# Optimization experiments

Hardware: AMD Instinct MI355X
Metric: run time of the kernel (lower is better)

The kernel has to match this reference:

```python
import jax, jax.numpy as jnp
import numpy as np

D = 1024
H = 16
HD = D // H
DS = 64
B, L = 2, 2048


def setup_inputs() -> dict:
    key = jax.random.key(0)
    ks = jax.random.split(key, 12)
    s = 0.02
    return {
        "x": jax.random.normal(ks[0], (B, L, D), jnp.float32),
        "subject_embed": jax.random.normal(ks[1], (B, DS), jnp.float32),
        "key_padding_mask": jnp.zeros((B, L), jnp.bool_),
        "Wq": jax.random.normal(ks[2], (D, D), jnp.float32) * s,
        "Wk": jax.random.normal(ks[3], (D, D), jnp.float32) * s,
        "Wv": jax.random.normal(ks[4], (D, D), jnp.float32) * s,
        "Wo": jax.random.normal(ks[5], (D, D), jnp.float32) * s,
        "bo": jnp.zeros((D,), jnp.float32),
        "Wsq": jax.random.normal(ks[6], (DS, D), jnp.float32) * s,
        "bsq": jnp.zeros((D,), jnp.float32),
        "Wsk": jax.random.normal(ks[7], (DS, D), jnp.float32) * s,
        "bsk": jnp.zeros((D,), jnp.float32),
    }


def reference(x, subject_embed, key_padding_mask, Wq, Wk, Wv, Wo, bo, Wsq, bsq, Wsk, bsk):
    scale = 1.0 / jnp.sqrt(jnp.asarray(HD, x.dtype))
    q = x @ Wq + (subject_embed @ Wsq + bsq)[:, None, :]   # [B,L,D]
    k = x @ Wk + (subject_embed @ Wsk + bsk)[:, None, :]
    v = x @ Wv
    # split heads: [B,H,L,hd]
    q = q.reshape(B, L, H, HD).transpose(0, 2, 1, 3)
    k = k.reshape(B, L, H, HD).transpose(0, 2, 1, 3)
    v = v.reshape(B, L, H, HD).transpose(0, 2, 1, 3)
    attn = jnp.einsum('bhqd,bhkd->bhqk', q, k) * scale      # [B,H,L,L]
    attn = jnp.where(key_padding_mask[:, None, None, :], -jnp.inf, attn)
    attn = jax.nn.softmax(attn, axis=-1)
    out = jnp.einsum('bhqk,bhkd->bhqd', attn, v)
    out = out.transpose(0, 2, 1, 3).reshape(B, L, D)
    return out @ Wo + bo
```

## Files before the change

### kernel.cpp

```cpp
#include <hip/hip_runtime.h>
#include <hip/hip_bf16.h>
#include <math.h>

#define DEV __device__ __forceinline__

typedef short bf16x8 __attribute__((ext_vector_type(8)));
typedef float f32x4 __attribute__((ext_vector_type(4)));

static constexpr int D  = 1024;
static constexpr int H  = 16;
static constexpr int HD = 64;
static constexpr int DS = 64;
static constexpr int B  = 2;
static constexpr int L  = 2048;
static constexpr int M  = B * L;

static constexpr float QSCALE = 0.18033688011112042f;

DEV unsigned short f2bf(float f) {
  union { float f; unsigned u; } x; x.f = f;
  unsigned r = (x.u + 0x7FFFu + ((x.u >> 16) & 1u)) >> 16;
  return (unsigned short)r;
}

DEV unsigned pack2bf(float a, float b) {
  return (unsigned)f2bf(a) | ((unsigned)f2bf(b) << 16);
}

DEV unsigned pack2bf_trunc(float a, float b) {
  union { float f; unsigned u; } ua{a}, ub{b};
  return (ua.u >> 16) | (ub.u & 0xffff0000u);
}

DEV void gload_lds16(const void* g, void* l) {
  __builtin_amdgcn_global_load_lds(
      (const __attribute__((address_space(1))) unsigned int*)g,
      (__attribute__((address_space(3))) unsigned int*)l, 16, 0, 0);
}

__global__ __launch_bounds__(256) void prep_kernel(
    const float* __restrict__ Wq, const float* __restrict__ Wk,
    const float* __restrict__ Wv, const float* __restrict__ Wo,
    const float* __restrict__ x, const float* __restrict__ subj,
    const float* __restrict__ Wsq, const float* __restrict__ bsq,
    const float* __restrict__ Wsk, const float* __restrict__ bsk,
    unsigned short* __restrict__ WT4, unsigned short* __restrict__ xb,
    float* __restrict__ sq, float* __restrict__ sk) {
  __shared__ float tile[64][65];
  const int blk = blockIdx.x, t = threadIdx.x;
  if (blk < 1024) {
    const int z = blk >> 8, idx = blk & 255;
    const float* W = z == 0 ? Wq : z == 1 ? Wk : z == 2 ? Wv : Wo;
    unsigned short* dst = WT4 + (size_t)z * D * D;
    const int n0 = (idx & 15) * 64, k0 = (idx >> 4) * 64;
    const int c = t & 63, r4 = t >> 6;
#pragma unroll
    for (int rr = 0; rr < 16; ++rr) {
      int row = r4 + rr * 4;
      tile[row][c] = W[(size_t)(k0 + row) * D + n0 + c];
    }
    __syncthreads();
#pragma unroll
    for (int rr = 0; rr < 16; ++rr) {
      int nrow = r4 + rr * 4;
      dst[(size_t)(n0 + nrow) * D + k0 + c] = f2bf(tile[c][nrow]);
    }
  } else if (blk < 3072) {
    size_t g = (size_t)(blk - 1024) * 256 + t;
    const float4* xf = (const float4*)x;
    float4 a = xf[2 * g], b = xf[2 * g + 1];
    union { unsigned short s[8]; uint4 v; } o;
    o.s[0] = f2bf(a.x); o.s[1] = f2bf(a.y); o.s[2] = f2bf(a.z); o.s[3] = f2bf(a.w);
    o.s[4] = f2bf(b.x); o.s[5] = f2bf(b.y); o.s[6] = f2bf(b.z); o.s[7] = f2bf(b.w);
    ((uint4*)xb)[g] = o.v;
  } else {
    int g = (blk - 3072) * 256 + t;
    int ty = g >> 11, b = (g >> 10) & 1, n = g & 1023;
    const float* W = ty ? Wsk : Wsq;
    const float* bias = ty ? bsk : bsq;
    float s = bias[n];
#pragma unroll 8
    for (int d = 0; d < DS; ++d) s += subj[b * DS + d] * W[d * D + n];
    (ty ? sk : sq)[b * D + n] = s;
  }
}

__global__ __launch_bounds__(256) void proj_kernel(
    const unsigned short* __restrict__ xb, const unsigned short* __restrict__ WT3,
    const float* __restrict__ sq, const float* __restrict__ sk,
    unsigned short* __restrict__ qk, unsigned short* __restrict__ vT) {
  __shared__ __align__(16) unsigned short smem[128 * 136];
  unsigned short* As = smem;
  unsigned short* Bs = smem + 128 * 64;
  const int z = blockIdx.z;
  const unsigned short* Wt = WT3 + (size_t)z * D * D;
  const int m0 = blockIdx.y * 128, n0 = blockIdx.x * 128;
  const int t = threadIdx.x, l = t & 63, w = t >> 6;
  const int wm = w >> 1, wn = w & 1;
  const int lm = l & 15, lq = l >> 4;
  const int srow8 = t >> 3;
  const int fsw = ((t & 7) ^ ((t >> 3) & 7)) * 8;
  const int swm = lm & 7;
  f32x4 acc[4][4] = {};
  for (int kt = 0; kt < D / 64; ++kt) {
    const int kb = kt * 64;
#pragma unroll
    for (int c = 0; c < 4; ++c) {
      int row = 32 * c + srow8;
      gload_lds16(&xb[(size_t)(m0 + row) * D + kb + fsw], &As[(32 * c + 8 * w) * 64]);
      gload_lds16(&Wt[(size_t)(n0 + row) * D + kb + fsw], &Bs[(32 * c + 8 * w) * 64]);
    }
    __syncthreads();
#pragma unroll
    for (int kk = 0; kk < 2; ++kk) {
      bf16x8 af[4], bf[4];
#pragma unroll
      for (int i = 0; i < 4; ++i)
        af[i] = *(const bf16x8*)&As[(64 * wm + 16 * i + lm) * 64 + ((kk * 4 + lq) ^ swm) * 8];
#pragma unroll
      for (int j = 0; j < 4; ++j)
        bf[j] = *(const bf16x8*)&Bs[(64 * wn + 16 * j + lm) * 64 + ((kk * 4 + lq) ^ swm) * 8];
#pragma unroll
      for (int i = 0; i < 4; ++i)
#pragma unroll
        for (int j = 0; j < 4; ++j)
          acc[i][j] = __builtin_amdgcn_mfma_f32_16x16x32_bf16(af[i], bf[j], acc[i][j], 0, 0, 0);
    }
    __syncthreads();
  }
  if (z == 2) {
#pragma unroll
    for (int i = 0; i < 4; ++i)
#pragma unroll
      for (int j = 0; j < 4; ++j) {
        int cr = 64 * wn + 16 * j + lm;
        int rr = 64 * wm + 16 * i + 4 * lq;
        uint2 u;
        u.x = pack2bf(acc[i][j][0], acc[i][j][1]);
        u.y = pack2bf(acc[i][j][2], acc[i][j][3]);
        *(uint2*)&smem[cr * 136 + rr] = u;
      }
    __syncthreads();
    const int cr = t >> 1, half = t & 1;
    const int bb = m0 >> 11, l0 = m0 & (L - 1);
    const int gcol = n0 + cr, h = gcol >> 6, hd = gcol & 63;
    size_t dbase = ((size_t)(bb * H + h) * HD + hd) * L + l0 + half * 64;
#pragma unroll
    for (int c = 0; c < 8; ++c) {
      uint4 u = *(const uint4*)&smem[cr * 136 + half * 64 + c * 8];
      *(uint4*)&vT[dbase + c * 8] = u;
    }
  } else {
    unsigned short* dst = qk + (size_t)z * M * D;
    const float* bias = z == 0 ? sq : sk;
    const float post = z == 0 ? QSCALE : 1.0f;
#pragma unroll
    for (int i = 0; i < 4; ++i)
#pragma unroll
      for (int j = 0; j < 4; ++j)
#pragma unroll
        for (int r = 0; r < 4; ++r) {
          int grow = m0 + 64 * wm + 16 * i + lq * 4 + r;
          int gcol = n0 + 64 * wn + 16 * j + lm;
          int bb = grow >> 11, ll = grow & (L - 1);
          float v = (acc[i][j][r] + bias[bb * D + gcol]) * post;
          int h = gcol >> 6, hd = gcol & 63;
          dst[((size_t)(bb * H + h) * L + ll) * HD + hd] = f2bf(v);
        }
  }
}

__global__ __launch_bounds__(256) void attn_kernel(
    const unsigned short* __restrict__ q_hm, const unsigned short* __restrict__ k_hm,
    const unsigned short* __restrict__ vT, const unsigned char* __restrict__ mask,
    unsigned short* __restrict__ ctx) {
  __shared__ unsigned short Ksb[2 * 64 * 64];
  __shared__ unsigned short Vtb[2 * 64 * 64];
  __shared__ unsigned short Ps[128 * 72];
  const int bx = blockIdx.x;
  const int rest = bx >> 3;
  const int bhid = (bx & 7) + 8 * (rest >> 4);
  const int q0 = (rest & 15) * 128;
  const int h = bhid & 15, b = bhid >> 4;
  const size_t bh = (size_t)(b * H + h);
  const unsigned short* qp = q_hm + bh * L * HD;
  const unsigned short* kp = k_hm + bh * L * HD;
  const unsigned short* vp = vT + bh * HD * L;
  const int t = threadIdx.x, l = t & 63, w = t >> 6;
  const int lm = l & 15, lq = l >> 4;
  const int fsw = ((t & 7) ^ ((t >> 3) & 7)) * 8;
  const int swm = lm & 7;
  const int srow = t >> 3;

  unsigned short* Qs = Ps;
#pragma unroll
  for (int c = 0; c < 4; ++c) {
    int row = 32 * c + srow;
    gload_lds16(&qp[(size_t)(q0 + row) * HD + fsw], &Qs[(32 * c + 8 * w) * 64]);
  }
#pragma unroll
  for (int c = 0; c < 2; ++c) {
    int row = 32 * c + srow;
    gload_lds16(&kp[(size_t)row * HD + fsw], &Ksb[(32 * c + 8 * w) * 64]);
    gload_lds16(&vp[(size_t)row * L + fsw], &Vtb[(32 * c + 8 * w) * 64]);
  }
  __syncthreads();
  bf16x8 qf[2][2];
#pragma unroll
  for (int i = 0; i < 2; ++i)
#pragma unroll
    for (int kk = 0; kk < 2; ++kk)
      qf[i][kk] = *(const bf16x8*)&Qs[(w * 32 + 16 * i + lm) * 64 + ((kk * 4 + lq) ^ swm) * 8];

  float lsum[2] = {0.f, 0.f};
  f32x4 ot[4][2] = {};

  for (int kt = 0; kt < L / 64; ++kt) {
    const int cur = kt & 1;
    const unsigned short* Kc = Ksb + cur * (64 * 64);
    const unsigned short* Vc = Vtb + cur * (64 * 64);
    if (kt + 1 < L / 64) {
      const int nk0 = (kt + 1) * 64;
      unsigned short* Kd = Ksb + (cur ^ 1) * (64 * 64);
      unsigned short* Vd = Vtb + (cur ^ 1) * (64 * 64);
#pragma unroll
      for (int c = 0; c < 2; ++c) {
        int row = 32 * c + srow;
        gload_lds16(&kp[(size_t)(nk0 + row) * HD + fsw], &Kd[(32 * c + 8 * w) * 64]);
        gload_lds16(&vp[(size_t)row * L + nk0 + fsw], &Vd[(32 * c + 8 * w) * 64]);
      }
    }
    unsigned long long mb = __ballot(mask[b * L + kt * 64 + l] != 0);

    f32x4 st[4][2];
#pragma unroll
    for (int jt = 0; jt < 4; ++jt) {
      bf16x8 kf[2];
#pragma unroll
      for (int kk = 0; kk < 2; ++kk)
        kf[kk] = *(const bf16x8*)&Kc[(16 * jt + lm) * 64 + ((kk * 4 + lq) ^ swm) * 8];
#pragma unroll
      for (int i = 0; i < 2; ++i) {
        f32x4 a = {};
        a = __builtin_amdgcn_mfma_f32_16x16x32_bf16(kf[0], qf[i][0], a, 0, 0, 0);
        a = __builtin_amdgcn_mfma_f32_16x16x32_bf16(kf[1], qf[i][1], a, 0, 0, 0);
        st[jt][i] = a;
      }
    }
    if (mb) {
      unsigned mlo = (unsigned)(mb >> (4 * lq));
      unsigned mhi = (unsigned)(mb >> (4 * lq + 32));
#pragma unroll
      for (int jt = 0; jt < 4; ++jt)
#pragma unroll
        for (int i = 0; i < 2; ++i)
#pragma unroll
          for (int r = 0; r < 4; ++r) {
            unsigned bits = jt < 2 ? mlo : mhi;
            if ((bits >> (16 * (jt & 1) + r)) & 1u) st[jt][i][r] = -1e30f;
          }
    }
#pragma unroll
    for (int i = 0; i < 2; ++i) {
      float ps = 0.f;
#pragma unroll
      for (int jt = 0; jt < 4; ++jt) {
        f32x4 p;
#pragma unroll
        for (int r = 0; r < 4; ++r) {
          float e = __builtin_amdgcn_exp2f(st[jt][i][r]);
          p[r] = e;
          ps += e;
        }
        uint2 u;
        u.x = pack2bf_trunc(p[0], p[1]);
        u.y = pack2bf_trunc(p[2], p[3]);
        *(uint2*)&Ps[(w * 32 + 16 * i + lm) * 72 + 16 * jt + 4 * lq] = u;
      }
      lsum[i] += ps;
    }
    bf16x8 pf[2][2];
#pragma unroll
    for (int i = 0; i < 2; ++i)
#pragma unroll
      for (int kk = 0; kk < 2; ++kk)
        pf[i][kk] = *(const bf16x8*)&Ps[(w * 32 + 16 * i + lm) * 72 + kk * 32 + lq * 8];
#pragma unroll
    for (int jf = 0; jf < 4; ++jf) {
      bf16x8 vf[2];
#pragma unroll
      for (int kk = 0; kk < 2; ++kk)
        vf[kk] = *(const bf16x8*)&Vc[(16 * jf + lm) * 64 + ((kk * 4 + lq) ^ swm) * 8];
#pragma unroll
      for (int i = 0; i < 2; ++i) {
        ot[jf][i] = __builtin_amdgcn_mfma_f32_16x16x32_bf16(vf[0], pf[i][0], ot[jf][i], 0, 0, 0);
        ot[jf][i] = __builtin_amdgcn_mfma_f32_16x16x32_bf16(vf[1], pf[i][1], ot[jf][i], 0, 0, 0);
      }
    }
    __syncthreads();
  }

  float rl[2];
#pragma unroll
  for (int i = 0; i < 2; ++i) {
    float s = lsum[i];
    s += __shfl_xor(s, 16, 64);
    s += __shfl_xor(s, 32, 64);
    rl[i] = 1.0f / s;
  }

#pragma unroll
  for (int i = 0; i < 2; ++i) {
#pragma unroll
    for (int jf = 0; jf < 4; ++jf) {
      uint2 u;
      u.x = pack2bf(ot[jf][i][0] * rl[i], ot[jf][i][1] * rl[i]);
      u.y = pack2bf(ot[jf][i][2] * rl[i], ot[jf][i][3] * rl[i]);
      *(uint2*)&Ps[(w * 32 + 16 * i + lm) * 72 + 16 * jf + 4 * lq] = u;
    }
  }
  {
    int row = l >> 1, half = l & 1;
    size_t obase = ((size_t)(b * L + q0 + w * 32 + row)) * D + h * HD + half * 32;
#pragma unroll
    for (int c = 0; c < 4; ++c) {
      uint4 u = *(const uint4*)&Ps[(w * 32 + row) * 72 + half * 32 + c * 8];
      *(uint4*)&ctx[obase + c * 8] = u;
    }
  }
}

__global__ __launch_bounds__(256) void outgemm_kernel(
    const unsigned short* __restrict__ ctx, const unsigned short* __restrict__ WoT,
    const float* __restrict__ bo, float* __restrict__ out) {
  __shared__ unsigned short As[64 * 64];
  __shared__ unsigned short Bs[128 * 64];
  const int m0 = blockIdx.y * 64, n0 = blockIdx.x * 128;
  const int t = threadIdx.x, l = t & 63, w = t >> 6;
  const int wm = w >> 1, wn = w & 1;
  const int lm = l & 15, lq = l >> 4;
  const int srow8 = t >> 3;
  const int fsw = ((t & 7) ^ ((t >> 3) & 7)) * 8;
  const int swm = lm & 7;
  f32x4 acc[2][4] = {};
  for (int kt = 0; kt < D / 64; ++kt) {
    const int kb = kt * 64;
#pragma unroll
    for (int c = 0; c < 2; ++c)
      gload_lds16(&ctx[(size_t)(m0 + 32 * c + srow8) * D + kb + fsw],
                  &As[(32 * c + 8 * w) * 64]);
#pragma unroll
    for (int c = 0; c < 4; ++c)
      gload_lds16(&WoT[(size_t)(n0 + 32 * c + srow8) * D + kb + fsw],
                  &Bs[(32 * c + 8 * w) * 64]);
    __syncthreads();
#pragma unroll
    for (int kk = 0; kk < 2; ++kk) {
      bf16x8 af[2], bf[4];
#pragma unroll
      for (int i = 0; i < 2; ++i)
        af[i] = *(const bf16x8*)&As[(32 * wm + 16 * i + lm) * 64 + ((kk * 4 + lq) ^ swm) * 8];
#pragma unroll
      for (int j = 0; j < 4; ++j)
        bf[j] = *(const bf16x8*)&Bs[(64 * wn + 16 * j + lm) * 64 + ((kk * 4 + lq) ^ swm) * 8];
#pragma unroll
      for (int i = 0; i < 2; ++i)
#pragma unroll
        for (int j = 0; j < 4; ++j)
          acc[i][j] = __builtin_amdgcn_mfma_f32_16x16x32_bf16(af[i], bf[j], acc[i][j], 0, 0, 0);
    }
    __syncthreads();
  }
#pragma unroll
  for (int i = 0; i < 2; ++i)
#pragma unroll
    for (int j = 0; j < 4; ++j)
#pragma unroll
      for (int r = 0; r < 4; ++r) {
        int grow = m0 + 32 * wm + 16 * i + lq * 4 + r;
        int gcol = n0 + 64 * wn + 16 * j + lm;
        out[(size_t)grow * D + gcol] = acc[i][j][r] + bo[gcol];
      }
}

extern "C" void kernel_launch(void* const* d_in, const int* in_sizes, int n_in,
                              void* d_out, int out_size, void* d_ws, size_t ws_size,
                              hipStream_t stream) {
  const float* x    = (const float*)d_in[0];
  const float* subj = (const float*)d_in[1];
  const unsigned char* mask = (const unsigned char*)d_in[2];
  const float* Wq = (const float*)d_in[3];
  const float* Wk = (const float*)d_in[4];
  const float* Wv = (const float*)d_in[5];
  const float* Wo = (const float*)d_in[6];
  const float* bo = (const float*)d_in[7];
  const float* Wsq = (const float*)d_in[8];
  const float* bsq = (const float*)d_in[9];
  const float* Wsk = (const float*)d_in[10];
  const float* bsk = (const float*)d_in[11];
  float* out = (float*)d_out;
  char* ws = (char*)d_ws;

  unsigned short* xb  = (unsigned short*)(ws);
  unsigned short* WT4 = (unsigned short*)(ws + (8ull  << 20));
  unsigned short* qk  = (unsigned short*)(ws + (16ull << 20));
  unsigned short* ctx = (unsigned short*)(ws + (32ull << 20));
  unsigned short* vT  = (unsigned short*)(ws + (40ull << 20));
  float* sq = (float*)(ws + (48ull << 20));
  float* sk = sq + B * D;

  hipLaunchKernelGGL(prep_kernel, dim3(3088), dim3(256), 0, stream,
                     Wq, Wk, Wv, Wo, x, subj, Wsq, bsq, Wsk, bsk, WT4, xb, sq, sk);
  hipLaunchKernelGGL(proj_kernel, dim3(8, 32, 3), dim3(256), 0, stream,
                     xb, WT4, sq, sk, qk, vT);
  hipLaunchKernelGGL(attn_kernel, dim3(512), dim3(256), 0, stream,
                     qk, qk + (size_t)M * D, vT, mask, ctx);
  hipLaunchKernelGGL(outgemm_kernel, dim3(8, 64, 1), dim3(256), 0, stream, ctx,
                     WT4 + 3ull * D * D, bo, out);
}
```

Before: 218.8 us.

## Split attention KV range in two and merge partials in a reduce kernel

The attention kernel now splits each query tile's key range into two halves, doubling the grid so more blocks are resident per CU. Each half writes unnormalized bf16 partial outputs and row sums to workspace. A new reduce kernel adds the two partials, normalizes them and writes the context tensor. This costs extra global traffic for the partials, an extra launch, and some precision from storing unnormalized partials in bf16.

```diff
diff --git a/kernel.cpp b/kernel.cpp
--- a/kernel.cpp
+++ b/kernel.cpp
@@ -21,6 +21,10 @@
   union { float f; unsigned u; } x; x.f = f;
   unsigned r = (x.u + 0x7FFFu + ((x.u >> 16) & 1u)) >> 16;
   return (unsigned short)r;
+}
+
+DEV float bf2f(unsigned short s) {
+  union { unsigned u; float f; } x; x.u = (unsigned)s << 16; return x.f;
 }
 
 DEV unsigned pack2bf(float a, float b) {
@@ -173,16 +177,19 @@
 __global__ __launch_bounds__(256) void attn_kernel(
     const unsigned short* __restrict__ q_hm, const unsigned short* __restrict__ k_hm,
     const unsigned short* __restrict__ vT, const unsigned char* __restrict__ mask,
-    unsigned short* __restrict__ ctx) {
+    unsigned short* __restrict__ opart, float* __restrict__ lsp) {
   __shared__ unsigned short Ksb[2 * 64 * 64];
   __shared__ unsigned short Vtb[2 * 64 * 64];
   __shared__ unsigned short Ps[128 * 72];
   const int bx = blockIdx.x;
   const int rest = bx >> 3;
-  const int bhid = (bx & 7) + 8 * (rest >> 4);
-  const int q0 = (rest & 15) * 128;
+  const int bhid = (bx & 7) + 8 * (rest >> 5);
+  const int qs = rest & 31;
+  const int q0 = (qs >> 1) * 128;
+  const int split = qs & 1;
   const int h = bhid & 15, b = bhid >> 4;
   const size_t bh = (size_t)(b * H + h);
+  const int slot = ((bhid * 16 + (qs >> 1)) * 2 + split);
   const unsigned short* qp = q_hm + bh * L * HD;
   const unsigned short* kp = k_hm + bh * L * HD;
   const unsigned short* vp = vT + bh * HD * L;
@@ -191,6 +198,7 @@
   const int fsw = ((t & 7) ^ ((t >> 3) & 7)) * 8;
   const int swm = lm & 7;
   const int srow = t >> 3;
+  const int kt0 = split * (L / 128), kt1 = kt0 + L / 128;
 
   unsigned short* Qs = Ps;
 #pragma unroll
@@ -201,8 +209,8 @@
 #pragma unroll
   for (int c = 0; c < 2; ++c) {
     int row = 32 * c + srow;
-    gload_lds16(&kp[(size_t)row * HD + fsw], &Ksb[(32 * c + 8 * w) * 64]);
-    gload_lds16(&vp[(size_t)row * L + fsw], &Vtb[(32 * c + 8 * w) * 64]);
+    gload_lds16(&kp[(size_t)(kt0 * 64 + row) * HD + fsw], &Ksb[(32 * c + 8 * w) * 64]);
+    gload_lds16(&vp[(size_t)row * L + kt0 * 64 + fsw], &Vtb[(32 * c + 8 * w) * 64]);
   }
   __syncthreads();
   bf16x8 qf[2][2];
@@ -215,11 +223,11 @@
   float lsum[2] = {0.f, 0.f};
   f32x4 ot[4][2] = {};
 
-  for (int kt = 0; kt < L / 64; ++kt) {
+  for (int kt = kt0; kt < kt1; ++kt) {
     const int cur = kt & 1;
     const unsigned short* Kc = Ksb + cur * (64 * 64);
     const unsigned short* Vc = Vtb + cur * (64 * 64);
-    if (kt + 1 < L / 64) {
+    if (kt + 1 < kt1) {
       const int nk0 = (kt + 1) * 64;
       unsigned short* Kd = Ksb + (cur ^ 1) * (64 * 64);
       unsigned short* Vd = Vtb + (cur ^ 1) * (64 * 64);
@@ -300,33 +308,47 @@
     __syncthreads();
   }
 
-  float rl[2];
+  unsigned short* op = opart + (size_t)slot * (128 * 64);
 #pragma unroll
   for (int i = 0; i < 2; ++i) {
     float s = lsum[i];
     s += __shfl_xor(s, 16, 64);
     s += __shfl_xor(s, 32, 64);
-    rl[i] = 1.0f / s;
-  }
-
-#pragma unroll
-  for (int i = 0; i < 2; ++i) {
 #pragma unroll
     for (int jf = 0; jf < 4; ++jf) {
       uint2 u;
-      u.x = pack2bf(ot[jf][i][0] * rl[i], ot[jf][i][1] * rl[i]);
-      u.y = pack2bf(ot[jf][i][2] * rl[i], ot[jf][i][3] * rl[i]);
-      *(uint2*)&Ps[(w * 32 + 16 * i + lm) * 72 + 16 * jf + 4 * lq] = u;
-    }
-  }
-  {
-    int row = l >> 1, half = l & 1;
-    size_t obase = ((size_t)(b * L + q0 + w * 32 + row)) * D + h * HD + half * 32;
-#pragma unroll
-    for (int c = 0; c < 4; ++c) {
-      uint4 u = *(const uint4*)&Ps[(w * 32 + row) * 72 + half * 32 + c * 8];
-      *(uint4*)&ctx[obase + c * 8] = u;
-    }
+      u.x = pack2bf(ot[jf][i][0], ot[jf][i][1]);
+      u.y = pack2bf(ot[jf][i][2], ot[jf][i][3]);
+      *(uint2*)&op[(w * 32 + 16 * i + lm) * 64 + 16 * jf + 4 * lq] = u;
+    }
+    if (l < 16) lsp[slot * 128 + w * 32 + 16 * i + l] = s;
+  }
+}
+
+__global__ __launch_bounds__(256) void reduce_kernel(
+    const unsigned short* __restrict__ opart, const float* __restrict__ lsp,
+    unsigned short* __restrict__ ctx) {
+  const int qt = blockIdx.x, bh = blockIdx.y;
+  const int t = threadIdx.x, row = t >> 1, half = t & 1;
+  const int slot = (bh * 16 + qt) * 2;
+  const unsigned short* o0 = opart + (size_t)slot * (128 * 64);
+  const unsigned short* o1 = o0 + 128 * 64;
+  const float rl = 1.0f / (lsp[slot * 128 + row] + lsp[(slot + 1) * 128 + row]);
+  const int b = bh >> 4, h = bh & 15;
+  size_t cb = ((size_t)(b * L + qt * 128 + row)) * D + h * 64 + half * 32;
+#pragma unroll
+  for (int c = 0; c < 4; ++c) {
+    int off = row * 64 + half * 32 + c * 8;
+    union { uint4 v; unsigned short s[8]; } u0, u1, o;
+    u0.v = *(const uint4*)&o0[off];
+    u1.v = *(const uint4*)&o1[off];
+#pragma unroll
+    for (int e = 0; e < 8; e += 2) {
+      float a = (bf2f(u0.s[e]) + bf2f(u1.s[e])) * rl;
+      float bb2 = (bf2f(u0.s[e + 1]) + bf2f(u1.s[e + 1])) * rl;
+      ((unsigned*)&o.v)[e >> 1] = pack2bf(a, bb2);
+    }
+    *(uint4*)&ctx[cb + c * 8] = o.v;
   }
 }
 
@@ -401,20 +423,24 @@
   float* out = (float*)d_out;
   char* ws = (char*)d_ws;
 
-  unsigned short* xb  = (unsigned short*)(ws);
-  unsigned short* WT4 = (unsigned short*)(ws + (8ull  << 20));
-  unsigned short* qk  = (unsigned short*)(ws + (16ull << 20));
-  unsigned short* ctx = (unsigned short*)(ws + (32ull << 20));
-  unsigned short* vT  = (unsigned short*)(ws + (40ull << 20));
-  float* sq = (float*)(ws + (48ull << 20));
-  float* sk = sq + B * D;
+  unsigned short* xb    = (unsigned short*)(ws);
+  unsigned short* WT4   = (unsigned short*)(ws + (8ull  << 20));
+  unsigned short* qk    = (unsigned short*)(ws + (16ull << 20));
+  unsigned short* ctx   = (unsigned short*)(ws + (32ull << 20));
+  unsigned short* vT    = (unsigned short*)(ws + (40ull << 20));
+  float* sq             = (float*)(ws + (48ull << 20));
+  float* sk             = sq + B * D;
+  unsigned short* opart = (unsigned short*)(ws + (49ull << 20));
+  float* lsp            = (float*)(ws + (65ull << 20));
 
   hipLaunchKernelGGL(prep_kernel, dim3(3088), dim3(256), 0, stream,
                      Wq, Wk, Wv, Wo, x, subj, Wsq, bsq, Wsk, bsk, WT4, xb, sq, sk);
   hipLaunchKernelGGL(proj_kernel, dim3(8, 32, 3), dim3(256), 0, stream,
                      xb, WT4, sq, sk, qk, vT);
-  hipLaunchKernelGGL(attn_kernel, dim3(512), dim3(256), 0, stream,
-                     qk, qk + (size_t)M * D, vT, mask, ctx);
+  hipLaunchKernelGGL(attn_kernel, dim3(1024), dim3(256), 0, stream,
+                     qk, qk + (size_t)M * D, vT, mask, opart, lsp);
+  hipLaunchKernelGGL(reduce_kernel, dim3(16, 32), dim3(256), 0, stream,
+                     opart, lsp, ctx);
   hipLaunchKernelGGL(outgemm_kernel, dim3(8, 64, 1), dim3(256), 0, stream, ctx,
                      WT4 + 3ull * D * D, bo, out);
 }
```

New measurement: 228.3 us. 4.3% more time.

## Keep softmax probabilities in registers for PV MFMA and stage Q/K epilogue via LDS

Applied to the files above, without the earlier changes.

The attention PV product now uses 16x16x16 bf16 MFMA with the probability tile taken straight from registers as the A operand. This removes the per-tile LDS write and read-back of P, with the output accumulator transposed to match. The Q/K projection epilogue now stages results in shared memory and writes coalesced 16-byte rows in head-major layout instead of scattered 2-byte stores. The trade-off is twice as many smaller MFMA instructions and narrower V loads from LDS, plus an extra barrier in the GEMM epilogue.

```diff
diff --git a/kernel.cpp b/kernel.cpp
--- a/kernel.cpp
+++ b/kernel.cpp
@@ -5,7 +5,14 @@
 #define DEV __device__ __forceinline__
 
 typedef short bf16x8 __attribute__((ext_vector_type(8)));
+typedef short bf16x4 __attribute__((ext_vector_type(4)));
 typedef float f32x4 __attribute__((ext_vector_type(4)));
+
+#if __has_builtin(__builtin_amdgcn_mfma_f32_16x16x16bf16_1k)
+#define HAVE_MFMA16 1
+#else
+#define HAVE_MFMA16 0
+#endif
 
 static constexpr int D  = 1024;
 static constexpr int H  = 16;
@@ -160,13 +167,21 @@
       for (int j = 0; j < 4; ++j)
 #pragma unroll
         for (int r = 0; r < 4; ++r) {
-          int grow = m0 + 64 * wm + 16 * i + lq * 4 + r;
-          int gcol = n0 + 64 * wn + 16 * j + lm;
-          int bb = grow >> 11, ll = grow & (L - 1);
-          float v = (acc[i][j][r] + bias[bb * D + gcol]) * post;
-          int h = gcol >> 6, hd = gcol & 63;
-          dst[((size_t)(bb * H + h) * L + ll) * HD + hd] = f2bf(v);
+          int rr = 64 * wm + 16 * i + 4 * lq + r;
+          int cc = 64 * wn + 16 * j + lm;
+          float v = (acc[i][j][r] + bias[((m0 + rr) >> 11) * D + n0 + cc]) * post;
+          smem[rr * 136 + cc] = f2bf(v);
         }
+    __syncthreads();
+    const int row = t >> 1, half = t & 1;
+    const int bb = m0 >> 11, ll = (m0 & (L - 1)) + row;
+    const int h0 = (n0 >> 6) + half;
+    size_t dbase = ((size_t)(bb * H + h0) * L + ll) * HD;
+#pragma unroll
+    for (int c = 0; c < 8; ++c) {
+      uint4 u = *(const uint4*)&smem[row * 136 + half * 64 + c * 8];
+      *(uint4*)&dst[dbase + c * 8] = u;
+    }
   }
 }
 
@@ -213,7 +228,7 @@
       qf[i][kk] = *(const bf16x8*)&Qs[(w * 32 + 16 * i + lm) * 64 + ((kk * 4 + lq) ^ swm) * 8];
 
   float lsum[2] = {0.f, 0.f};
-  f32x4 ot[4][2] = {};
+  f32x4 ot[2][4] = {};
 
   for (int kt = 0; kt < L / 64; ++kt) {
     const int cur = kt & 1;
@@ -260,6 +275,9 @@
             if ((bits >> (16 * (jt & 1) + r)) & 1u) st[jt][i][r] = -1e30f;
           }
     }
+#if HAVE_MFMA16
+    union { uint2 u; bf16x4 v; } pp[2][4];
+#endif
 #pragma unroll
     for (int i = 0; i < 2; ++i) {
       float ps = 0.f;
@@ -272,13 +290,32 @@
           p[r] = e;
           ps += e;
         }
+#if HAVE_MFMA16
+        pp[i][jt].u.x = pack2bf_trunc(p[0], p[1]);
+        pp[i][jt].u.y = pack2bf_trunc(p[2], p[3]);
+#else
         uint2 u;
         u.x = pack2bf_trunc(p[0], p[1]);
         u.y = pack2bf_trunc(p[2], p[3]);
         *(uint2*)&Ps[(w * 32 + 16 * i + lm) * 72 + 16 * jt + 4 * lq] = u;
+#endif
       }
       lsum[i] += ps;
     }
+#if HAVE_MFMA16
+#pragma unroll
+    for (int jf = 0; jf < 4; ++jf) {
+#pragma unroll
+      for (int kc = 0; kc < 4; ++kc) {
+        int chunk = (2 * kc + (lq >> 1)) ^ swm;
+        bf16x4 vb = *(const bf16x4*)&Vc[(16 * jf + lm) * 64 + chunk * 8 + 4 * (lq & 1)];
+#pragma unroll
+        for (int i = 0; i < 2; ++i)
+          ot[i][jf] = __builtin_amdgcn_mfma_f32_16x16x16bf16_1k(
+              pp[i][kc].v, vb, ot[i][jf], 0, 0, 0);
+      }
+    }
+#else
     bf16x8 pf[2][2];
 #pragma unroll
     for (int i = 0; i < 2; ++i)
@@ -293,10 +330,11 @@
         vf[kk] = *(const bf16x8*)&Vc[(16 * jf + lm) * 64 + ((kk * 4 + lq) ^ swm) * 8];
 #pragma unroll
       for (int i = 0; i < 2; ++i) {
-        ot[jf][i] = __builtin_amdgcn_mfma_f32_16x16x32_bf16(vf[0], pf[i][0], ot[jf][i], 0, 0, 0);
-        ot[jf][i] = __builtin_amdgcn_mfma_f32_16x16x32_bf16(vf[1], pf[i][1], ot[jf][i], 0, 0, 0);
-      }
-    }
+        ot[i][jf] = __builtin_amdgcn_mfma_f32_16x16x32_bf16(vf[0], pf[i][0], ot[i][jf], 0, 0, 0);
+        ot[i][jf] = __builtin_amdgcn_mfma_f32_16x16x32_bf16(vf[1], pf[i][1], ot[i][jf], 0, 0, 0);
+      }
+    }
+#endif
     __syncthreads();
   }
 
@@ -309,16 +347,30 @@
     rl[i] = 1.0f / s;
   }
 
+#if HAVE_MFMA16
 #pragma unroll
   for (int i = 0; i < 2; ++i) {
+    float rlq[4];
+#pragma unroll
+    for (int r = 0; r < 4; ++r) rlq[r] = __shfl(rl[i], 4 * lq + r, 64);
+#pragma unroll
+    for (int jf = 0; jf < 4; ++jf)
+#pragma unroll
+      for (int r = 0; r < 4; ++r)
+        Ps[(w * 32 + 16 * i + 4 * lq + r) * 72 + 16 * jf + lm] =
+            f2bf(ot[i][jf][r] * rlq[r]);
+  }
+#else
+#pragma unroll
+  for (int i = 0; i < 2; ++i)
 #pragma unroll
     for (int jf = 0; jf < 4; ++jf) {
       uint2 u;
-      u.x = pack2bf(ot[jf][i][0] * rl[i], ot[jf][i][1] * rl[i]);
-      u.y = pack2bf(ot[jf][i][2] * rl[i], ot[jf][i][3] * rl[i]);
+      u.x = pack2bf(ot[i][jf][0] * rl[i], ot[i][jf][1] * rl[i]);
+      u.y = pack2bf(ot[i][jf][2] * rl[i], ot[i][jf][3] * rl[i]);
       *(uint2*)&Ps[(w * 32 + 16 * i + lm) * 72 + 16 * jf + 4 * lq] = u;
     }
-  }
+#endif
   {
     int row = l >> 1, half = l & 1;
     size_t obase = ((size_t)(b * L + q0 + w * 32 + row)) * D + h * HD + half * 32;
```

Result: no change. 220.5 us (+0.8%).

## Keep softmax probabilities in registers for PV MFMA and widen key tiles

Applied to the files above, without the earlier changes.

The attention kernel now feeds the exp'd score fragments straight into a 16x16x16 MFMA as the A operand, which removes the LDS round-trip for P. Key tiles grow from 64 to 128 rows, halving the loop iterations and barriers, and the V tile layout and swizzle change to suit the new operand order. The QK projection epilogue also stages results through shared memory so head-major writes become coalesced 16-byte stores. The cost is more LDS per block (larger K/V double buffers), which may reduce occupancy, plus extra shuffles to redistribute the row normalisers in the epilogue.

```diff
diff --git a/kernel.cpp b/kernel.cpp
--- a/kernel.cpp
+++ b/kernel.cpp
@@ -5,6 +5,7 @@
 #define DEV __device__ __forceinline__
 
 typedef short bf16x8 __attribute__((ext_vector_type(8)));
+typedef short bf16x4 __attribute__((ext_vector_type(4)));
 typedef float f32x4 __attribute__((ext_vector_type(4)));
 
 static constexpr int D  = 1024;
@@ -160,13 +161,21 @@
       for (int j = 0; j < 4; ++j)
 #pragma unroll
         for (int r = 0; r < 4; ++r) {
-          int grow = m0 + 64 * wm + 16 * i + lq * 4 + r;
-          int gcol = n0 + 64 * wn + 16 * j + lm;
-          int bb = grow >> 11, ll = grow & (L - 1);
-          float v = (acc[i][j][r] + bias[bb * D + gcol]) * post;
-          int h = gcol >> 6, hd = gcol & 63;
-          dst[((size_t)(bb * H + h) * L + ll) * HD + hd] = f2bf(v);
+          int rr = 64 * wm + 16 * i + 4 * lq + r;
+          int cc = 64 * wn + 16 * j + lm;
+          float v = (acc[i][j][r] + bias[((m0 + rr) >> 11) * D + n0 + cc]) * post;
+          smem[rr * 136 + cc] = f2bf(v);
         }
+    __syncthreads();
+    const int row = t >> 1, half = t & 1;
+    const int bb = m0 >> 11, ll = (m0 & (L - 1)) + row;
+    const int h0 = (n0 >> 6) + half;
+    size_t dbase = ((size_t)(bb * H + h0) * L + ll) * HD;
+#pragma unroll
+    for (int c = 0; c < 8; ++c) {
+      uint4 u = *(const uint4*)&smem[row * 136 + half * 64 + c * 8];
+      *(uint4*)&dst[dbase + c * 8] = u;
+    }
   }
 }
 
@@ -174,9 +183,9 @@
     const unsigned short* __restrict__ q_hm, const unsigned short* __restrict__ k_hm,
     const unsigned short* __restrict__ vT, const unsigned char* __restrict__ mask,
     unsigned short* __restrict__ ctx) {
-  __shared__ unsigned short Ksb[2 * 64 * 64];
-  __shared__ unsigned short Vtb[2 * 64 * 64];
-  __shared__ unsigned short Ps[128 * 72];
+  __shared__ unsigned short Qs[128 * 64];
+  __shared__ unsigned short Ksb[2 * 128 * 64];
+  __shared__ unsigned short Vtb[2 * 64 * 128];
   const int bx = blockIdx.x;
   const int rest = bx >> 3;
   const int bhid = (bx & 7) + 8 * (rest >> 4);
@@ -191,18 +200,14 @@
   const int fsw = ((t & 7) ^ ((t >> 3) & 7)) * 8;
   const int swm = lm & 7;
   const int srow = t >> 3;
-
-  unsigned short* Qs = Ps;
+  const int vs = t & 15, vr = t >> 4;
+  const int vcsrc = ((vs & 8) | ((vs & 7) ^ (vr & 7))) * 8;
+
 #pragma unroll
   for (int c = 0; c < 4; ++c) {
-    int row = 32 * c + srow;
-    gload_lds16(&qp[(size_t)(q0 + row) * HD + fsw], &Qs[(32 * c + 8 * w) * 64]);
-  }
-#pragma unroll
-  for (int c = 0; c < 2; ++c) {
-    int row = 32 * c + srow;
-    gload_lds16(&kp[(size_t)row * HD + fsw], &Ksb[(32 * c + 8 * w) * 64]);
-    gload_lds16(&vp[(size_t)row * L + fsw], &Vtb[(32 * c + 8 * w) * 64]);
+    gload_lds16(&qp[(size_t)(q0 + 32 * c + srow) * HD + fsw], &Qs[(32 * c + 8 * w) * 64]);
+    gload_lds16(&kp[(size_t)(32 * c + srow) * HD + fsw], &Ksb[(32 * c + 8 * w) * 64]);
+    gload_lds16(&vp[(size_t)(16 * c + vr) * L + vcsrc], &Vtb[(16 * c + 4 * w) * 128]);
   }
   __syncthreads();
   bf16x8 qf[2][2];
@@ -213,88 +218,73 @@
       qf[i][kk] = *(const bf16x8*)&Qs[(w * 32 + 16 * i + lm) * 64 + ((kk * 4 + lq) ^ swm) * 8];
 
   float lsum[2] = {0.f, 0.f};
-  f32x4 ot[4][2] = {};
-
-  for (int kt = 0; kt < L / 64; ++kt) {
+  f32x4 ot[2][4] = {};
+
+  for (int kt = 0; kt < L / 128; ++kt) {
     const int cur = kt & 1;
-    const unsigned short* Kc = Ksb + cur * (64 * 64);
-    const unsigned short* Vc = Vtb + cur * (64 * 64);
-    if (kt + 1 < L / 64) {
-      const int nk0 = (kt + 1) * 64;
-      unsigned short* Kd = Ksb + (cur ^ 1) * (64 * 64);
-      unsigned short* Vd = Vtb + (cur ^ 1) * (64 * 64);
-#pragma unroll
-      for (int c = 0; c < 2; ++c) {
-        int row = 32 * c + srow;
-        gload_lds16(&kp[(size_t)(nk0 + row) * HD + fsw], &Kd[(32 * c + 8 * w) * 64]);
-        gload_lds16(&vp[(size_t)row * L + nk0 + fsw], &Vd[(32 * c + 8 * w) * 64]);
-      }
-    }
-    unsigned long long mb = __ballot(mask[b * L + kt * 64 + l] != 0);
-
-    f32x4 st[4][2];
-#pragma unroll
-    for (int jt = 0; jt < 4; ++jt) {
-      bf16x8 kf[2];
-#pragma unroll
-      for (int kk = 0; kk < 2; ++kk)
-        kf[kk] = *(const bf16x8*)&Kc[(16 * jt + lm) * 64 + ((kk * 4 + lq) ^ swm) * 8];
+    const unsigned short* Kc = Ksb + cur * (128 * 64);
+    const unsigned short* Vc = Vtb + cur * (64 * 128);
+    unsigned char mby0 = mask[b * L + kt * 128 + l];
+    unsigned char mby1 = mask[b * L + kt * 128 + 64 + l];
+    if (kt + 1 < L / 128) {
+      const int nk0 = (kt + 1) * 128;
+      unsigned short* Kd = Ksb + (cur ^ 1) * (128 * 64);
+      unsigned short* Vd = Vtb + (cur ^ 1) * (64 * 128);
+#pragma unroll
+      for (int c = 0; c < 4; ++c) {
+        gload_lds16(&kp[(size_t)(nk0 + 32 * c + srow) * HD + fsw], &Kd[(32 * c + 8 * w) * 64]);
+        gload_lds16(&vp[(size_t)(16 * c + vr) * L + nk0 + vcsrc], &Vd[(16 * c + 4 * w) * 128]);
+      }
+    }
+    unsigned long long mb0 = __ballot(mby0 != 0);
+    unsigned long long mb1 = __ballot(mby1 != 0);
+
+#pragma unroll
+    for (int jt = 0; jt < 8; ++jt) {
+      bf16x8 kf0 = *(const bf16x8*)&Kc[(16 * jt + lm) * 64 + ((0 + lq) ^ swm) * 8];
+      bf16x8 kf1 = *(const bf16x8*)&Kc[(16 * jt + lm) * 64 + ((4 + lq) ^ swm) * 8];
+      f32x4 st[2];
 #pragma unroll
       for (int i = 0; i < 2; ++i) {
         f32x4 a = {};
-        a = __builtin_amdgcn_mfma_f32_16x16x32_bf16(kf[0], qf[i][0], a, 0, 0, 0);
-        a = __builtin_amdgcn_mfma_f32_16x16x32_bf16(kf[1], qf[i][1], a, 0, 0, 0);
-        st[jt][i] = a;
-      }
-    }
-    if (mb) {
-      unsigned mlo = (unsigned)(mb >> (4 * lq));
-      unsigned mhi = (unsigned)(mb >> (4 * lq + 32));
-#pragma unroll
-      for (int jt = 0; jt < 4; ++jt)
+        a = __builtin_amdgcn_mfma_f32_16x16x32_bf16(kf0, qf[i][0], a, 0, 0, 0);
+        a = __builtin_amdgcn_mfma_f32_16x16x32_bf16(kf1, qf[i][1], a, 0, 0, 0);
+        st[i] = a;
+      }
+      unsigned long long mbX = jt < 4 ? mb0 : mb1;
+      if (mbX) {
+        int jm = jt & 3;
+        unsigned bits = (unsigned)(mbX >> (4 * lq + 16 * jm));
 #pragma unroll
         for (int i = 0; i < 2; ++i)
 #pragma unroll
-          for (int r = 0; r < 4; ++r) {
-            unsigned bits = jt < 2 ? mlo : mhi;
-            if ((bits >> (16 * (jt & 1) + r)) & 1u) st[jt][i][r] = -1e30f;
-          }
-    }
-#pragma unroll
-    for (int i = 0; i < 2; ++i) {
-      float ps = 0.f;
-#pragma unroll
-      for (int jt = 0; jt < 4; ++jt) {
+          for (int r = 0; r < 4; ++r)
+            if ((bits >> r) & 1u) st[i][r] = -1e30f;
+      }
+      union { uint2 u; bf16x4 v; } pp[2];
+#pragma unroll
+      for (int i = 0; i < 2; ++i) {
         f32x4 p;
+        float ps = 0.f;
 #pragma unroll
         for (int r = 0; r < 4; ++r) {
-          float e = __builtin_amdgcn_exp2f(st[jt][i][r]);
+          float e = __builtin_amdgcn_exp2f(st[i][r]);
           p[r] = e;
           ps += e;
         }
-        uint2 u;
-        u.x = pack2bf_trunc(p[0], p[1]);
-        u.y = pack2bf_trunc(p[2], p[3]);
-        *(uint2*)&Ps[(w * 32 + 16 * i + lm) * 72 + 16 * jt + 4 * lq] = u;
-      }
-      lsum[i] += ps;
-    }
-    bf16x8 pf[2][2];
-#pragma unroll
-    for (int i = 0; i < 2; ++i)
-#pragma unroll
-      for (int kk = 0; kk < 2; ++kk)
-        pf[i][kk] = *(const bf16x8*)&Ps[(w * 32 + 16 * i + lm) * 72 + kk * 32 + lq * 8];
-#pragma unroll
-    for (int jf = 0; jf < 4; ++jf) {
-      bf16x8 vf[2];
-#pragma unroll
-      for (int kk = 0; kk < 2; ++kk)
-        vf[kk] = *(const bf16x8*)&Vc[(16 * jf + lm) * 64 + ((kk * 4 + lq) ^ swm) * 8];
-#pragma unroll
-      for (int i = 0; i < 2; ++i) {
-        ot[jf][i] = __builtin_amdgcn_mfma_f32_16x16x32_bf16(vf[0], pf[i][0], ot[jf][i], 0, 0, 0);
-        ot[jf][i] = __builtin_amdgcn_mfma_f32_16x16x32_bf16(vf[1], pf[i][1], ot[jf][i], 0, 0, 0);
+        lsum[i] += ps;
+        pp[i].u.x = pack2bf_trunc(p[0], p[1]);
+        pp[i].u.y = pack2bf_trunc(p[2], p[3]);
+      }
+      const int kc2 = 2 * jt + (lq >> 1);
+      const int slot = (kc2 & 8) | ((kc2 & 7) ^ swm);
+#pragma unroll
+      for (int jf = 0; jf < 4; ++jf) {
+        bf16x4 vb = *(const bf16x4*)&Vc[(16 * jf + lm) * 128 + slot * 8 + 4 * (lq & 1)];
+#pragma unroll
+        for (int i = 0; i < 2; ++i)
+          ot[i][jf] = __builtin_amdgcn_mfma_f32_16x16x16bf16_1k(
+              pp[i].v, vb, ot[i][jf], 0, 0, 0);
       }
     }
     __syncthreads();
@@ -309,22 +299,25 @@
     rl[i] = 1.0f / s;
   }
 
+  unsigned short* Es = Ksb;
 #pragma unroll
   for (int i = 0; i < 2; ++i) {
-#pragma unroll
-    for (int jf = 0; jf < 4; ++jf) {
-      uint2 u;
-      u.x = pack2bf(ot[jf][i][0] * rl[i], ot[jf][i][1] * rl[i]);
-      u.y = pack2bf(ot[jf][i][2] * rl[i], ot[jf][i][3] * rl[i]);
-      *(uint2*)&Ps[(w * 32 + 16 * i + lm) * 72 + 16 * jf + 4 * lq] = u;
-    }
+    float rlq[4];
+#pragma unroll
+    for (int r = 0; r < 4; ++r) rlq[r] = __shfl(rl[i], 4 * lq + r, 64);
+#pragma unroll
+    for (int jf = 0; jf < 4; ++jf)
+#pragma unroll
+      for (int r = 0; r < 4; ++r)
+        Es[(w * 32 + 16 * i + 4 * lq + r) * 72 + 16 * jf + lm] =
+            f2bf(ot[i][jf][r] * rlq[r]);
   }
   {
     int row = l >> 1, half = l & 1;
     size_t obase = ((size_t)(b * L + q0 + w * 32 + row)) * D + h * HD + half * 32;
 #pragma unroll
     for (int c = 0; c < 4; ++c) {
-      uint4 u = *(const uint4*)&Ps[(w * 32 + row) * 72 + half * 32 + c * 8];
+      uint4 u = *(const uint4*)&Es[(w * 32 + row) * 72 + half * 32 + c * 8];
       *(uint4*)&ctx[obase + c * 8] = u;
     }
   }
```

New measurement: 214.3 us. 1.02x faster.
